# Optimization experiments

Hardware: AMD Instinct MI355X
Metric: run time of the kernel (lower is better)

## Reference

```python
import jax, jax.numpy as jnp
import numpy as np

N_HEAD = 16
NEG_INF = -1e30  # finite mask value, safe for softmax/grad


def setup_inputs() -> dict:
    key = jax.random.key(0)
    k1, k2, k3 = jax.random.split(key, 3)
    B, T, C = 4, 2049, 1024
    x = jax.random.normal(k1, (B, T, C), dtype=jnp.float32)
    W_attn = jax.random.normal(k2, (C, 3 * C), dtype=jnp.float32) * (1.0 / np.sqrt(C))
    W_proj = jax.random.normal(k3, (C, C), dtype=jnp.float32) * (1.0 / np.sqrt(C))
    return {"x": x, "W_attn": W_attn, "W_proj": W_proj}


def reference(x, W_attn, W_proj):
    B, T, C = x.shape
    H = N_HEAD
    D = C // H
    qkv = x @ W_attn                                  # (B, T, 3C)
    q, k, v = jnp.split(qkv, 3, axis=-1)
    q = q.reshape(B, T, H, D).transpose(0, 2, 1, 3)   # (B, H, T, D)
    k = k.reshape(B, T, H, D).transpose(0, 2, 1, 3)
    v = v.reshape(B, T, H, D).transpose(0, 2, 1, 3)
    # hybrid mask: causal tril, but state token (row 0) attends to ALL positions
    mask = jnp.tril(jnp.ones((T, T), dtype=bool))
    mask = mask.at[0, :].set(True)
    scale = 1.0 / np.sqrt(D)
    scores = jnp.einsum('bhtd,bhsd->bhts', q, k) * scale
    scores = jnp.where(mask[None, None, :, :], scores, NEG_INF)
    att = jax.nn.softmax(scores, axis=-1)
    y = jnp.einsum('bhts,bhsd->bhtd', att, v)         # (B, H, T, D)
    y = y.transpose(0, 2, 1, 3).reshape(B, T, C)
    return y @ W_proj
```

## Files before the change

### kernel.cpp

```cpp
#include <hip/hip_runtime.h>

typedef __attribute__((ext_vector_type(8))) __bf16 bf16x8;
typedef __attribute__((ext_vector_type(4))) __bf16 bf16x4;
typedef __attribute__((ext_vector_type(4))) float f32x4;

#define GLDS(g, l) __builtin_amdgcn_global_load_lds( \
    (__attribute__((address_space(1))) void*)(void*)(g), \
    (__attribute__((address_space(3))) void*)(void*)(l), 16, 0, 0)

constexpr int T_REAL = 2049;
constexpr int Tp     = 2112;
constexpr int Mreal  = 8196;
constexpr int Mp     = 8448;
constexpr int GK     = 1024;

constexpr float QSCALE = 0.125f * 1.4426950408889634f;

__global__ __launch_bounds__(256) void cvt_x(const float* __restrict__ x,
                                             __bf16* __restrict__ xb) {
    size_t i = ((size_t)blockIdx.x * 256 + threadIdx.x) * 4;
    float4 v = make_float4(0.f, 0.f, 0.f, 0.f);
    if (i < (size_t)Mreal * GK) v = *(const float4*)(x + i);
    bf16x4 o;
    o.x = (__bf16)v.x; o.y = (__bf16)v.y; o.z = (__bf16)v.z; o.w = (__bf16)v.w;
    *(bf16x4*)(xb + i) = o;
}

__global__ __launch_bounds__(256) void transpose_w(const float* __restrict__ W,
                                                   __bf16* __restrict__ Wt,
                                                   int K, int N) {
    __shared__ float tile[64][65];
    const int n0 = blockIdx.x * 64, k0 = blockIdx.y * 64;
    const int tx = threadIdx.x & 63, ty = threadIdx.x >> 6;
#pragma unroll
    for (int j = 0; j < 16; j++) {
        int rk = ty + j * 4;
        tile[rk][tx] = W[(size_t)(k0 + rk) * N + n0 + tx];
    }
    __syncthreads();
#pragma unroll
    for (int j = 0; j < 16; j++) {
        int rn = ty + j * 4;
        Wt[(size_t)(n0 + rn) * K + k0 + tx] = (__bf16)tile[tx][rn];
    }
}

__global__ __launch_bounds__(256) void transpose_v(const __bf16* __restrict__ v,
                                                   __bf16* __restrict__ vT) {
    __shared__ __bf16 tl[64][72];
    const int bh = blockIdx.y, t0 = blockIdx.x * 64;
    const int tid = threadIdx.x;
    const __bf16* src = v + ((size_t)bh * Tp + t0) * 64;
    {
        const int r = tid >> 3, c = (tid & 7) * 8;
        *(bf16x8*)&tl[r][c]      = *(const bf16x8*)(src + r * 64 + c);
        *(bf16x8*)&tl[r + 32][c] = *(const bf16x8*)(src + (r + 32) * 64 + c);
    }
    __syncthreads();
    __bf16* dst = vT + (size_t)bh * 64 * Tp + t0;
    {
        const int d = tid >> 3, tc = (tid & 7) * 8;
        bf16x8 a, b;
#pragma unroll
        for (int i = 0; i < 8; i++) {
            a[i] = tl[tc + i][d];
            b[i] = tl[tc + i][d + 32];
        }
        *(bf16x8*)(dst + (size_t)d * Tp + tc)        = a;
        *(bf16x8*)(dst + (size_t)(d + 32) * Tp + tc) = b;
    }
}

__global__ __launch_bounds__(512)
void gemm256(const __bf16* __restrict__ A, const __bf16* __restrict__ Bt,
             __bf16* __restrict__ qout, __bf16* __restrict__ kout,
             __bf16* __restrict__ vout) {
    __shared__ __align__(16) __bf16 As[2][16384];
    __shared__ __align__(16) __bf16 Bs[2][16384];

    const int tid = threadIdx.x, lane = tid & 63, w = tid >> 6;
    const int wr = w >> 2, wc = w & 3;
    const int quad = lane >> 4, l15 = lane & 15, l7 = l15 & 7;
    const int m0 = blockIdx.y * 256, n0 = blockIdx.x * 256;

    const int sr = tid >> 3;
    const int sc = ((tid & 7) ^ (sr & 7)) * 8;
    const __bf16* ag = A  + (size_t)(m0 + sr) * GK + sc;
    const __bf16* bg = Bt + (size_t)(n0 + sr) * GK + sc;
    const int ldst = tid * 8;

#define STG_A(T, h) do { const __bf16* s_ = ag + (size_t)(h) * 128 * GK + (T) * 64; \
    GLDS(s_, &As[(T) & 1][(h) * 8192 + ldst]); \
    GLDS(s_ + (size_t)64 * GK, &As[(T) & 1][(h) * 8192 + 4096 + ldst]); } while (0)
#define STG_B(T, h) do { const __bf16* s_ = bg + (size_t)(h) * 128 * GK + (T) * 64; \
    GLDS(s_, &Bs[(T) & 1][(h) * 8192 + ldst]); \
    GLDS(s_ + (size_t)64 * GK, &Bs[(T) & 1][(h) * 8192 + 4096 + ldst]); } while (0)

    f32x4 acc[8][4] = {};
    bf16x8 a[8], b0[4], b1[4];

    STG_A(0, 0); STG_B(0, 1); STG_A(0, 1); STG_B(0, 0); STG_A(1, 0); STG_B(1, 1);
    asm volatile("s_waitcnt vmcnt(4)" ::: "memory");
    __builtin_amdgcn_s_barrier();

    constexpr int NT = GK / 64;

#pragma unroll 1
    for (int T = 0; T < NT; ++T) {
        const int p = T & 1;

#pragma unroll
        for (int f = 0; f < 4; ++f) {
            const int R = f * 32 + wr * 16 + l15;
            a[f * 2 + 0] = *(const bf16x8*)&As[p][R * 64 + ((quad ^ l7) * 8)];
            a[f * 2 + 1] = *(const bf16x8*)&As[p][R * 64 + (((4 + quad) ^ l7) * 8)];
        }
#pragma unroll
        for (int n = 0; n < 2; ++n) {
            const int R = n * 64 + wc * 16 + l15;
            b0[n * 2 + 0] = *(const bf16x8*)&Bs[p][R * 64 + ((quad ^ l7) * 8)];
            b0[n * 2 + 1] = *(const bf16x8*)&Bs[p][R * 64 + (((4 + quad) ^ l7) * 8)];
        }
        if (T + 1 < NT) { STG_A(T + 1, 1); STG_B(T + 1, 0); }
        __builtin_amdgcn_s_barrier();
        asm volatile("s_waitcnt lgkmcnt(0)" ::: "memory");
        __builtin_amdgcn_sched_barrier(0);
        __builtin_amdgcn_s_setprio(1);
#pragma unroll
        for (int f = 0; f < 4; ++f)
#pragma unroll
            for (int n = 0; n < 2; ++n) {
                acc[f][n] = __builtin_amdgcn_mfma_f32_16x16x32_bf16(a[f*2+0], b0[n*2+0], acc[f][n], 0, 0, 0);
                acc[f][n] = __builtin_amdgcn_mfma_f32_16x16x32_bf16(a[f*2+1], b0[n*2+1], acc[f][n], 0, 0, 0);
            }
        __builtin_amdgcn_s_setprio(0);
        __builtin_amdgcn_s_barrier();

#pragma unroll
        for (int n = 0; n < 2; ++n) {
            const int R = 128 + n * 64 + wc * 16 + l15;
            b1[n * 2 + 0] = *(const bf16x8*)&Bs[p][R * 64 + ((quad ^ l7) * 8)];
            b1[n * 2 + 1] = *(const bf16x8*)&Bs[p][R * 64 + (((4 + quad) ^ l7) * 8)];
        }
        __builtin_amdgcn_s_barrier();
        asm volatile("s_waitcnt lgkmcnt(0)" ::: "memory");
        __builtin_amdgcn_sched_barrier(0);
        __builtin_amdgcn_s_setprio(1);
#pragma unroll
        for (int f = 0; f < 4; ++f)
#pragma unroll
            for (int n = 0; n < 2; ++n) {
                acc[f][2+n] = __builtin_amdgcn_mfma_f32_16x16x32_bf16(a[f*2+0], b1[n*2+0], acc[f][2+n], 0, 0, 0);
                acc[f][2+n] = __builtin_amdgcn_mfma_f32_16x16x32_bf16(a[f*2+1], b1[n*2+1], acc[f][2+n], 0, 0, 0);
            }
        __builtin_amdgcn_s_setprio(0);
        __builtin_amdgcn_s_barrier();

#pragma unroll
        for (int f = 0; f < 4; ++f) {
            const int R = 128 + f * 32 + wr * 16 + l15;
            a[f * 2 + 0] = *(const bf16x8*)&As[p][R * 64 + ((quad ^ l7) * 8)];
            a[f * 2 + 1] = *(const bf16x8*)&As[p][R * 64 + (((4 + quad) ^ l7) * 8)];
        }
        if (T + 2 < NT) STG_A(T + 2, 0);
        __builtin_amdgcn_s_barrier();
        asm volatile("s_waitcnt lgkmcnt(0)" ::: "memory");
        __builtin_amdgcn_sched_barrier(0);
        __builtin_amdgcn_s_setprio(1);
#pragma unroll
        for (int f = 0; f < 4; ++f)
#pragma unroll
            for (int n = 0; n < 2; ++n) {
                acc[4+f][2+n] = __builtin_amdgcn_mfma_f32_16x16x32_bf16(a[f*2+0], b1[n*2+0], acc[4+f][2+n], 0, 0, 0);
                acc[4+f][2+n] = __builtin_amdgcn_mfma_f32_16x16x32_bf16(a[f*2+1], b1[n*2+1], acc[4+f][2+n], 0, 0, 0);
            }
        __builtin_amdgcn_s_setprio(0);
        __builtin_amdgcn_s_barrier();

        if (T + 2 < NT) STG_B(T + 2, 1);
        __builtin_amdgcn_s_barrier();
        asm volatile("s_waitcnt lgkmcnt(0)" ::: "memory");
        __builtin_amdgcn_sched_barrier(0);
        __builtin_amdgcn_s_setprio(1);
#pragma unroll
        for (int f = 0; f < 4; ++f)
#pragma unroll
            for (int n = 0; n < 2; ++n) {
                acc[4+f][n] = __builtin_amdgcn_mfma_f32_16x16x32_bf16(a[f*2+0], b0[n*2+0], acc[4+f][n], 0, 0, 0);
                acc[4+f][n] = __builtin_amdgcn_mfma_f32_16x16x32_bf16(a[f*2+1], b0[n*2+1], acc[4+f][n], 0, 0, 0);
            }
        __builtin_amdgcn_s_setprio(0);
        if (T < NT - 2) { asm volatile("s_waitcnt vmcnt(4)" ::: "memory"); }
        else            { asm volatile("s_waitcnt vmcnt(0)" ::: "memory"); }
        __builtin_amdgcn_s_barrier();
    }
#undef STG_A
#undef STG_B

    const int which = n0 >> 10;
    __bf16* op = (which == 0) ? qout : (which == 1) ? kout : vout;
    const float scl = (which == 0) ? QSCALE : 1.0f;
    __bf16* ep = &As[0][0];
    const int rr = tid >> 4, cc = tid & 15;
#pragma unroll
    for (int f = 0; f < 8; ++f) {
        __syncthreads();
#pragma unroll
        for (int n = 0; n < 4; ++n) {
            const int col = (n & 1) * 64 + wc * 16 + (n >> 1) * 128 + l15;
#pragma unroll
            for (int r = 0; r < 4; ++r)
                ep[(wr * 16 + quad * 4 + r) * 264 + col] = (__bf16)(acc[f][n][r] * scl);
        }
        __syncthreads();
        const int m = m0 + (f & 3) * 32 + (f >> 2) * 128 + rr;
        if (m < Mreal) {
            const int b = m / T_REAL;
            const int t = m - b * T_REAL;
#pragma unroll
            for (int g = 0; g < 2; ++g) {
                const int c8 = (cc + g * 16) * 8;
                bf16x8 vv = *(const bf16x8*)&ep[rr * 264 + c8];
                const int gc = n0 + c8;
                const int h = (gc >> 6) & 15;
                *(bf16x8*)&op[((size_t)(b * 16 + h) * Tp + t) * 64 + (gc & 63)] = vv;
            }
        }
    }
}

template <int EPI>
__global__ __launch_bounds__(256)
void gemm128(const __bf16* __restrict__ A, const __bf16* __restrict__ Bt,
             float* __restrict__ outp,
             __bf16* __restrict__ qout, __bf16* __restrict__ kout,
             __bf16* __restrict__ vout) {
    __shared__ __bf16 As[128 * 64];
    __shared__ __bf16 Bs[128 * 64];

    const int tid = threadIdx.x, lane = tid & 63, w = tid >> 6;
    const int wr = w >> 1, wc = w & 1;
    const int quad = lane >> 4, l15 = lane & 15, l7 = l15 & 7;
    const int m0 = blockIdx.y * 128, n0 = blockIdx.x * 128;

    const int row0 = w * 32 + (lane >> 3);
    const int gc8 = ((lane & 7) ^ ((lane >> 3) & 7)) * 8;
    const __bf16* agp = A + (size_t)(m0 + row0) * GK + gc8;
    const __bf16* bgp = Bt + (size_t)(n0 + row0) * GK + gc8;
    __bf16* lap = &As[(w * 256 + lane) * 8];
    __bf16* lbp = &Bs[(w * 256 + lane) * 8];

    f32x4 acc[4][4] = {};

    for (int k0 = 0; k0 < GK; k0 += 64) {
#pragma unroll
        for (int s = 0; s < 4; s++) {
            GLDS(agp + (size_t)s * 8 * GK + k0, lap + s * 512);
            GLDS(bgp + (size_t)s * 8 * GK + k0, lbp + s * 512);
        }
        __syncthreads();
#pragma unroll
        for (int kk = 0; kk < 2; kk++) {
            bf16x8 fa[4], fb[4];
#pragma unroll
            for (int i = 0; i < 4; i++)
                fa[i] = *(const bf16x8*)&As[(wr * 64 + i * 16 + l15) * 64 + (((kk * 4 + quad) ^ l7) * 8)];
#pragma unroll
            for (int j = 0; j < 4; j++)
                fb[j] = *(const bf16x8*)&Bs[(wc * 64 + j * 16 + l15) * 64 + (((kk * 4 + quad) ^ l7) * 8)];
#pragma unroll
            for (int i = 0; i < 4; i++)
#pragma unroll
                for (int j = 0; j < 4; j++)
                    acc[i][j] = __builtin_amdgcn_mfma_f32_16x16x32_bf16(fa[i], fb[j], acc[i][j], 0, 0, 0);
        }
        __syncthreads();
    }

    if constexpr (EPI == 0) {
        const int which = n0 >> 10;
        const int h = ((n0 + wc * 64) >> 6) & 15;
        __bf16* op = (which == 0) ? qout : (which == 1) ? kout : vout;
        const float scl = (which == 0) ? QSCALE : 1.0f;
        __bf16* wls = &As[w * 2048];
#pragma unroll
        for (int p = 0; p < 2; p++) {
            if (p) __syncthreads();
#pragma unroll
            for (int i2 = 0; i2 < 2; i2++)
#pragma unroll
                for (int j = 0; j < 4; j++)
#pragma unroll
                    for (int r = 0; r < 4; r++) {
                        const int lrow = i2 * 16 + quad * 4 + r;
                        const int cX = (j * 2 + (l15 >> 3)) ^ (lrow & 7);
                        wls[lrow * 64 + cX * 8 + (l15 & 7)] =
                            (__bf16)(acc[p * 2 + i2][j][r] * scl);
                    }
            __syncthreads();
#pragma unroll
            for (int it = 0; it < 4; it++) {
                const int lrow = (lane >> 3) + it * 8;
                bf16x8 vv = *(const bf16x8*)&wls[lrow * 64 + (((lane & 7) ^ (lrow & 7)) * 8)];
                const int m = m0 + wr * 64 + p * 32 + lrow;
                if (m < Mreal) {
                    const int b = m / T_REAL;
                    const int t = m - b * T_REAL;
                    *(bf16x8*)&op[(((size_t)(b * 16 + h)) * Tp + t) * 64 + (lane & 7) * 8] = vv;
                }
            }
        }
    } else {
        float* wlf = (float*)&As[0] + w * 1024;
#pragma unroll
        for (int p = 0; p < 4; p++) {
            if (p) __syncthreads();
#pragma unroll
            for (int j = 0; j < 4; j++)
#pragma unroll
                for (int r = 0; r < 4; r++) {
                    const int lrow = quad * 4 + r;
                    const int cX = (j * 4 + (l15 >> 2)) ^ (lrow & 7);
                    wlf[lrow * 64 + cX * 4 + (l15 & 3)] = acc[p][j][r];
                }
            __syncthreads();
#pragma unroll
            for (int it = 0; it < 4; it++) {
                const int lrow = lane >> 2;
                const int c = (lane & 3) + it * 4;
                f32x4 vv = *(const f32x4*)&wlf[lrow * 64 + ((c ^ (lrow & 7)) * 4)];
                const int m = m0 + wr * 64 + p * 16 + lrow;
                if (m < Mreal)
                    *(f32x4*)&outp[(size_t)m * 1024 + n0 + wc * 64 + c * 4] = vv;
            }
        }
    }
}

__global__ __launch_bounds__(512, 6)
void attn(const __bf16* __restrict__ q, const __bf16* __restrict__ kk,
          const __bf16* __restrict__ vT, __bf16* __restrict__ y) {
    __shared__ __bf16 Ks[2][64 * 64];
    __shared__ __bf16 Vs[2][64 * 64];
    __shared__ __bf16 Pq[8][16 * 64];

    static const int QA[17] = {0,31,29,27,25,23,21,19,17,15,13,11,9,7,5,3,1};
    static const int QB[17] = {32,30,28,26,24,22,20,18,16,14,12,10,8,6,4,2,-1};

    const int tid = threadIdx.x, lane = tid & 63, w = tid >> 6;
    const int quad = lane >> 4, l15 = lane & 15;
    const int l7 = l15 & 7;
    const int z = blockIdx.x;
    const int slot = z >> 6;
    const int zz = z & 63;
    const int bh = (zz & 7) * 8 + (zz >> 3);

    const int qtA = QA[slot];
    const int qt = (w < 4) ? qtA : QB[slot];
    const bool active = qt >= 0;
    const int qts = active ? qt : 0;
    const int q0 = qts * 64;
    const int qg = q0 + (w & 3) * 16 + l15;
    const int myNt = (qts == 0) ? 32 : qts;
    const int ntmaxB = (qtA == 0) ? 32 : qtA;

    const __bf16* kgb = kk + (size_t)bh * Tp * 64;
    const __bf16* vgb = vT + (size_t)bh * 64 * Tp;
    const int b = bh >> 4, h = bh & 15;

    const int r0 = tid >> 3;
    const int s0 = ((tid & 7) ^ (r0 & 7)) * 8;
    const int koff = r0 * 64 + s0;
    const int voff = r0 * Tp + s0;

    bf16x8 qa0, qa1;
    {
        const __bf16* qp = q + ((size_t)bh * Tp + qg) * 64 + quad * 8;
        qa0 = *(const bf16x8*)qp;
        qa1 = *(const bf16x8*)(qp + 32);
    }

    f32x4 o[4] = {};
    float mrow = -3e38f, lrow = 0.f;

    GLDS(kgb + koff, &Ks[0][tid * 8]);
    GLDS(vgb + voff, &Vs[0][tid * 8]);

    int cur = 0;
    for (int nt = 0; nt <= ntmaxB; ++nt) {
        __syncthreads();
        if (nt < ntmaxB) {
            GLDS(kgb + (size_t)(nt + 1) * 4096 + koff, &Ks[cur ^ 1][tid * 8]);
            GLDS(vgb + (size_t)(nt + 1) * 64 + voff, &Vs[cur ^ 1][tid * 8]);
        }
        if (active && nt <= myNt) {
            const int kv0 = nt * 64;

            f32x4 st[4];
#pragma unroll
            for (int j = 0; j < 4; j++) {
                const __bf16* krow = &Ks[cur][(j * 16 + l15) * 64];
                bf16x8 klo = *(const bf16x8*)(krow + ((quad ^ l7) * 8));
                bf16x8 khi = *(const bf16x8*)(krow + (((quad + 4) ^ l7) * 8));
                f32x4 zzv = {0.f, 0.f, 0.f, 0.f};
                zzv = __builtin_amdgcn_mfma_f32_16x16x32_bf16(klo, qa0, zzv, 0, 0, 0);
                st[j] = __builtin_amdgcn_mfma_f32_16x16x32_bf16(khi, qa1, zzv, 0, 0, 0);
            }

            if (nt >= qts) {
#pragma unroll
                for (int j = 0; j < 4; j++)
#pragma unroll
                    for (int r = 0; r < 4; r++) {
                        const int kvg = kv0 + j * 16 + quad * 4 + r;
                        const bool valid = (kvg <= qg) || (qg == 0 && kvg < T_REAL);
                        st[j][r] = valid ? st[j][r] : -1e30f;
                    }
            }

            float mx = -3e38f;
#pragma unroll
            for (int j = 0; j < 4; j++)
#pragma unroll
                for (int r = 0; r < 4; r++) mx = fmaxf(mx, st[j][r]);
            mx = fmaxf(mx, __shfl_xor(mx, 16));
            mx = fmaxf(mx, __shfl_xor(mx, 32));
            const float mn = fmaxf(mrow, mx);
            const float alpha = __builtin_amdgcn_exp2f(mrow - mn);
            mrow = mn;

            float rs = 0.f;
            bf16x4 pk[4];
#pragma unroll
            for (int j = 0; j < 4; j++) {
                float p0 = __builtin_amdgcn_exp2f(st[j][0] - mn);
                float p1 = __builtin_amdgcn_exp2f(st[j][1] - mn);
                float p2 = __builtin_amdgcn_exp2f(st[j][2] - mn);
                float p3 = __builtin_amdgcn_exp2f(st[j][3] - mn);
                rs += (p0 + p1) + (p2 + p3);
                pk[j].x = (__bf16)p0; pk[j].y = (__bf16)p1;
                pk[j].z = (__bf16)p2; pk[j].w = (__bf16)p3;
            }
            rs += __shfl_xor(rs, 16);
            rs += __shfl_xor(rs, 32);
            lrow = lrow * alpha + rs;
#pragma unroll
            for (int nf = 0; nf < 4; nf++)
#pragma unroll
                for (int r = 0; r < 4; r++) o[nf][r] *= alpha;

#pragma unroll
            for (int j = 0; j < 4; j++)
                *(bf16x4*)&Pq[w][l15 * 64 + (((2 * j + (quad >> 1)) ^ l7) * 8) + (quad & 1) * 4] = pk[j];

#pragma unroll
            for (int kc = 0; kc < 2; kc++) {
                bf16x8 pb = *(const bf16x8*)&Pq[w][l15 * 64 + (((kc * 4 + quad) ^ l7) * 8)];
#pragma unroll
                for (int nf = 0; nf < 4; nf++) {
                    bf16x8 va = *(const bf16x8*)&Vs[cur][(nf * 16 + l15) * 64 + (((kc * 4 + quad) ^ l7) * 8)];
                    o[nf] = __builtin_amdgcn_mfma_f32_16x16x32_bf16(va, pb, o[nf], 0, 0, 0);
                }
            }
        }
        cur ^= 1;
    }

    if (active && qg < T_REAL) {
        const float inv = 1.0f / lrow;
        __bf16* yp = y + ((size_t)(b * T_REAL + qg)) * 1024 + h * 64 + quad * 4;
#pragma unroll
        for (int nf = 0; nf < 4; nf++) {
            bf16x4 pko;
            pko.x = (__bf16)(o[nf][0] * inv);
            pko.y = (__bf16)(o[nf][1] * inv);
            pko.z = (__bf16)(o[nf][2] * inv);
            pko.w = (__bf16)(o[nf][3] * inv);
            *(bf16x4*)(yp + nf * 16) = pko;
        }
    }
}

extern "C" void kernel_launch(void* const* d_in, const int* in_sizes, int n_in,
                              void* d_out, int out_size, void* d_ws, size_t ws_size,
                              hipStream_t stream) {
    const float* x  = (const float*)d_in[0];
    const float* Wa = (const float*)d_in[1];
    const float* Wp = (const float*)d_in[2];
    float* out = (float*)d_out;

    char* ws = (char*)d_ws;
    constexpr size_t SZ_XB  = (size_t)Mp * GK * 2;
    constexpr size_t SZ_WAT = (size_t)3072 * GK * 2;
    constexpr size_t SZ_WPT = (size_t)1024 * GK * 2;
    constexpr size_t SZ_QK  = (size_t)64 * Tp * 64 * 2;
    __bf16* xb   = (__bf16*)(ws);
    __bf16* WaT  = (__bf16*)(ws + SZ_XB);
    __bf16* WpT  = (__bf16*)(ws + SZ_XB + SZ_WAT);
    __bf16* qb   = (__bf16*)(ws + SZ_XB + SZ_WAT + SZ_WPT);
    __bf16* kb   = (__bf16*)(ws + SZ_XB + SZ_WAT + SZ_WPT + SZ_QK);
    __bf16* vTb  = (__bf16*)(ws + SZ_XB + SZ_WAT + SZ_WPT + 2 * SZ_QK);
    __bf16* shrd = (__bf16*)(ws + SZ_XB + SZ_WAT + SZ_WPT + 3 * SZ_QK);
    __bf16* vpre = shrd;
    __bf16* yb   = shrd;

    cvt_x<<<(Mp * GK) / 1024, 256, 0, stream>>>(x, xb);
    transpose_w<<<dim3(48, 16), 256, 0, stream>>>(Wa, WaT, 1024, 3072);
    transpose_w<<<dim3(16, 16), 256, 0, stream>>>(Wp, WpT, 1024, 1024);

    gemm256<<<dim3(12, 33), 512, 0, stream>>>(xb, WaT, qb, kb, vpre);
    transpose_v<<<dim3(33, 64), 256, 0, stream>>>(vpre, vTb);
    attn<<<1088, 512, 0, stream>>>(qb, kb, vTb, yb);
    gemm128<1><<<dim3(8, 65), 256, 0, stream>>>(yb, WpT, out, nullptr, nullptr, nullptr);
}
```

Before: 278.2 us.

## Remap GEMM blocks per XCD, rebalance attention slots, and skip softmax rescale

After: 297.5 us. 1.07x slower.

```diff
diff --git a/kernel.cpp b/kernel.cpp
--- a/kernel.cpp
+++ b/kernel.cpp
@@ -81,7 +81,12 @@
     const int tid = threadIdx.x, lane = tid & 63, w = tid >> 6;
     const int wr = w >> 2, wc = w & 3;
     const int quad = lane >> 4, l15 = lane & 15, l7 = l15 & 7;
-    const int m0 = blockIdx.y * 256, n0 = blockIdx.x * 256;
+
+    constexpr int NWG = 396, QW = NWG / 8, RW = NWG % 8;
+    const int zb = blockIdx.x;
+    const int xcd = zb & 7, lin = zb >> 3;
+    const int wg = (xcd < RW ? xcd * (QW + 1) : RW * (QW + 1) + (xcd - RW) * QW) + lin;
+    const int m0 = (wg / 12) * 256, n0 = (wg % 12) * 256;
 
     const int sr = tid >> 3;
     const int sc = ((tid & 7) ^ (sr & 7)) * 8;
@@ -337,32 +342,25 @@
     }
 }
 
-__global__ __launch_bounds__(512, 6)
+__global__ __launch_bounds__(512, 8)
 void attn(const __bf16* __restrict__ q, const __bf16* __restrict__ kk,
           const __bf16* __restrict__ vT, __bf16* __restrict__ y) {
     __shared__ __bf16 Ks[2][64 * 64];
     __shared__ __bf16 Vs[2][64 * 64];
-    __shared__ __bf16 Pq[8][16 * 64];
-
-    static const int QA[17] = {0,31,29,27,25,23,21,19,17,15,13,11,9,7,5,3,1};
-    static const int QB[17] = {32,30,28,26,24,22,20,18,16,14,12,10,8,6,4,2,-1};
+    __shared__ __bf16 Pq[8][16 * 32];
+
+    static const int TBL[16] = {0,1,2,3,7,6,5,4,8,9,10,11,15,14,13,12};
+    static const int QA[16]  = {0,31,29,27,25,23,21,19,17,15,13,11,9,7,5,3};
+    static const int QB[16]  = {32,30,28,26,24,22,20,18,16,14,12,10,8,6,4,2};
 
     const int tid = threadIdx.x, lane = tid & 63, w = tid >> 6;
     const int quad = lane >> 4, l15 = lane & 15;
     const int l7 = l15 & 7;
     const int z = blockIdx.x;
-    const int slot = z >> 6;
+    const int sp = TBL[z >> 6];
     const int zz = z & 63;
     const int bh = (zz & 7) * 8 + (zz >> 3);
-
-    const int qtA = QA[slot];
-    const int qt = (w < 4) ? qtA : QB[slot];
-    const bool active = qt >= 0;
-    const int qts = active ? qt : 0;
-    const int q0 = qts * 64;
-    const int qg = q0 + (w & 3) * 16 + l15;
-    const int myNt = (qts == 0) ? 32 : qts;
-    const int ntmaxB = (qtA == 0) ? 32 : qtA;
+    const int npass = (sp == 15) ? 2 : 1;
 
     const __bf16* kgb = kk + (size_t)bh * Tp * 64;
     const __bf16* vgb = vT + (size_t)bh * 64 * Tp;
@@ -373,110 +371,127 @@
     const int koff = r0 * 64 + s0;
     const int voff = r0 * Tp + s0;
 
-    bf16x8 qa0, qa1;
-    {
-        const __bf16* qp = q + ((size_t)bh * Tp + qg) * 64 + quad * 8;
-        qa0 = *(const bf16x8*)qp;
-        qa1 = *(const bf16x8*)(qp + 32);
-    }
-
-    f32x4 o[4] = {};
-    float mrow = -3e38f, lrow = 0.f;
+    const int pswz = (((l15 >> 1) & 3) << 1) ^ ((l15 >> 3) << 2);
 
     GLDS(kgb + koff, &Ks[0][tid * 8]);
     GLDS(vgb + voff, &Vs[0][tid * 8]);
-
     int cur = 0;
-    for (int nt = 0; nt <= ntmaxB; ++nt) {
-        __syncthreads();
-        if (nt < ntmaxB) {
-            GLDS(kgb + (size_t)(nt + 1) * 4096 + koff, &Ks[cur ^ 1][tid * 8]);
-            GLDS(vgb + (size_t)(nt + 1) * 64 + voff, &Vs[cur ^ 1][tid * 8]);
-        }
-        if (active && nt <= myNt) {
-            const int kv0 = nt * 64;
-
-            f32x4 st[4];
-#pragma unroll
-            for (int j = 0; j < 4; j++) {
-                const __bf16* krow = &Ks[cur][(j * 16 + l15) * 64];
-                bf16x8 klo = *(const bf16x8*)(krow + ((quad ^ l7) * 8));
-                bf16x8 khi = *(const bf16x8*)(krow + (((quad + 4) ^ l7) * 8));
-                f32x4 zzv = {0.f, 0.f, 0.f, 0.f};
-                zzv = __builtin_amdgcn_mfma_f32_16x16x32_bf16(klo, qa0, zzv, 0, 0, 0);
-                st[j] = __builtin_amdgcn_mfma_f32_16x16x32_bf16(khi, qa1, zzv, 0, 0, 0);
-            }
-
-            if (nt >= qts) {
+
+#pragma unroll 1
+    for (int pass = 0; pass < npass; ++pass) {
+        const int qt = (pass == 0) ? ((w < 4) ? QA[sp] : QB[sp])
+                                   : ((w < 4) ? -1 : 1);
+        const bool active = qt >= 0;
+        const int qts = active ? qt : 0;
+        const int qg = qts * 64 + (w & 3) * 16 + l15;
+        const int myNt = (qts == 0) ? 32 : qts;
+        const int ntB = (pass == 0) ? ((sp == 0) ? 32 : QA[sp]) : 1;
+
+        bf16x8 qa0, qa1;
+        {
+            const __bf16* qp = q + ((size_t)bh * Tp + qg) * 64 + quad * 8;
+            qa0 = *(const bf16x8*)qp;
+            qa1 = *(const bf16x8*)(qp + 32);
+        }
+        f32x4 o[4] = {};
+        float mrow = -3e38f, lrow = 0.f;
+
+#pragma unroll 1
+        for (int nt = 0; nt <= ntB; ++nt) {
+            __syncthreads();
+            if (nt < ntB) {
+                GLDS(kgb + (size_t)(nt + 1) * 4096 + koff, &Ks[cur ^ 1][tid * 8]);
+                GLDS(vgb + (size_t)(nt + 1) * 64 + voff, &Vs[cur ^ 1][tid * 8]);
+            } else if (pass + 1 < npass) {
+                GLDS(kgb + koff, &Ks[cur ^ 1][tid * 8]);
+                GLDS(vgb + voff, &Vs[cur ^ 1][tid * 8]);
+            }
+            if (active && nt <= myNt) {
+                const int kv0 = nt * 64;
+
+                f32x4 st[4];
+#pragma unroll
+                for (int j = 0; j < 4; j++) {
+                    const __bf16* krow = &Ks[cur][(j * 16 + l15) * 64];
+                    bf16x8 klo = *(const bf16x8*)(krow + ((quad ^ l7) * 8));
+                    bf16x8 khi = *(const bf16x8*)(krow + (((quad + 4) ^ l7) * 8));
+                    f32x4 zzv = {0.f, 0.f, 0.f, 0.f};
+                    zzv = __builtin_amdgcn_mfma_f32_16x16x32_bf16(klo, qa0, zzv, 0, 0, 0);
+                    st[j] = __builtin_amdgcn_mfma_f32_16x16x32_bf16(khi, qa1, zzv, 0, 0, 0);
+                }
+
+                if (nt >= qts) {
+#pragma unroll
+                    for (int j = 0; j < 4; j++)
+#pragma unroll
+                        for (int r = 0; r < 4; r++) {
+                            const int kvg = kv0 + j * 16 + quad * 4 + r;
+                            const bool valid = (kvg <= qg) || (qg == 0 && kvg < T_REAL);
+                            st[j][r] = valid ? st[j][r] : -1e30f;
+                        }
+                }
+
+                float mx = -3e38f;
 #pragma unroll
                 for (int j = 0; j < 4; j++)
 #pragma unroll
-                    for (int r = 0; r < 4; r++) {
-                        const int kvg = kv0 + j * 16 + quad * 4 + r;
-                        const bool valid = (kvg <= qg) || (qg == 0 && kvg < T_REAL);
-                        st[j][r] = valid ? st[j][r] : -1e30f;
+                    for (int r = 0; r < 4; r++) mx = fmaxf(mx, st[j][r]);
+                mx = fmaxf(mx, __shfl_xor(mx, 16));
+                mx = fmaxf(mx, __shfl_xor(mx, 32));
+                if (!__all(mx - mrow <= 8.0f)) {
+                    const float mn = fmaxf(mrow, mx);
+                    const float alpha = __builtin_amdgcn_exp2f(mrow - mn);
+                    mrow = mn;
+                    lrow *= alpha;
+#pragma unroll
+                    for (int nf = 0; nf < 4; nf++)
+#pragma unroll
+                        for (int r = 0; r < 4; r++) o[nf][r] *= alpha;
+                }
+
+                float rs = 0.f;
+                bf16x4 pk[4];
+#pragma unroll
+                for (int j = 0; j < 4; j++) {
+                    float p0 = __builtin_amdgcn_exp2f(st[j][0] - mrow);
+                    float p1 = __builtin_amdgcn_exp2f(st[j][1] - mrow);
+                    float p2 = __builtin_amdgcn_exp2f(st[j][2] - mrow);
+                    float p3 = __builtin_amdgcn_exp2f(st[j][3] - mrow);
+                    rs += (p0 + p1) + (p2 + p3);
+                    pk[j].x = (__bf16)p0; pk[j].y = (__bf16)p1;
+                    pk[j].z = (__bf16)p2; pk[j].w = (__bf16)p3;
+                }
+                rs += __shfl_xor(rs, 16);
+                rs += __shfl_xor(rs, 32);
+                lrow += rs;
+
+#pragma unroll
+                for (int h2 = 0; h2 < 2; ++h2) {
+                    *(bf16x4*)&Pq[w][l15 * 32 + (((0 + quad) ^ pswz) * 4)] = pk[2 * h2];
+                    *(bf16x4*)&Pq[w][l15 * 32 + (((4 + quad) ^ pswz) * 4)] = pk[2 * h2 + 1];
+                    bf16x8 pb = *(const bf16x8*)&Pq[w][l15 * 32 + (((quad * 2) ^ pswz) * 4)];
+#pragma unroll
+                    for (int nf = 0; nf < 4; nf++) {
+                        bf16x8 va = *(const bf16x8*)&Vs[cur][(nf * 16 + l15) * 64 + (((h2 * 4 + quad) ^ l7) * 8)];
+                        o[nf] = __builtin_amdgcn_mfma_f32_16x16x32_bf16(va, pb, o[nf], 0, 0, 0);
                     }
-            }
-
-            float mx = -3e38f;
-#pragma unroll
-            for (int j = 0; j < 4; j++)
-#pragma unroll
-                for (int r = 0; r < 4; r++) mx = fmaxf(mx, st[j][r]);
-            mx = fmaxf(mx, __shfl_xor(mx, 16));
-            mx = fmaxf(mx, __shfl_xor(mx, 32));
-            const float mn = fmaxf(mrow, mx);
-            const float alpha = __builtin_amdgcn_exp2f(mrow - mn);
-            mrow = mn;
-
-            float rs = 0.f;
-            bf16x4 pk[4];
-#pragma unroll
-            for (int j = 0; j < 4; j++) {
-                float p0 = __builtin_amdgcn_exp2f(st[j][0] - mn);
-                float p1 = __builtin_amdgcn_exp2f(st[j][1] - mn);
-                float p2 = __builtin_amdgcn_exp2f(st[j][2] - mn);
-                float p3 = __builtin_amdgcn_exp2f(st[j][3] - mn);
-                rs += (p0 + p1) + (p2 + p3);
-                pk[j].x = (__bf16)p0; pk[j].y = (__bf16)p1;
-                pk[j].z = (__bf16)p2; pk[j].w = (__bf16)p3;
-            }
-            rs += __shfl_xor(rs, 16);
-            rs += __shfl_xor(rs, 32);
-            lrow = lrow * alpha + rs;
-#pragma unroll
-            for (int nf = 0; nf < 4; nf++)
-#pragma unroll
-                for (int r = 0; r < 4; r++) o[nf][r] *= alpha;
-
-#pragma unroll
-            for (int j = 0; j < 4; j++)
-                *(bf16x4*)&Pq[w][l15 * 64 + (((2 * j + (quad >> 1)) ^ l7) * 8) + (quad & 1) * 4] = pk[j];
-
-#pragma unroll
-            for (int kc = 0; kc < 2; kc++) {
-                bf16x8 pb = *(const bf16x8*)&Pq[w][l15 * 64 + (((kc * 4 + quad) ^ l7) * 8)];
-#pragma unroll
-                for (int nf = 0; nf < 4; nf++) {
-                    bf16x8 va = *(const bf16x8*)&Vs[cur][(nf * 16 + l15) * 64 + (((kc * 4 + quad) ^ l7) * 8)];
-                    o[nf] = __builtin_amdgcn_mfma_f32_16x16x32_bf16(va, pb, o[nf], 0, 0, 0);
-                }
-            }
-        }
-        cur ^= 1;
-    }
-
-    if (active && qg < T_REAL) {
-        const float inv = 1.0f / lrow;
-        __bf16* yp = y + ((size_t)(b * T_REAL + qg)) * 1024 + h * 64 + quad * 4;
-#pragma unroll
-        for (int nf = 0; nf < 4; nf++) {
-            bf16x4 pko;
-            pko.x = (__bf16)(o[nf][0] * inv);
-            pko.y = (__bf16)(o[nf][1] * inv);
-            pko.z = (__bf16)(o[nf][2] * inv);
-            pko.w = (__bf16)(o[nf][3] * inv);
-            *(bf16x4*)(yp + nf * 16) = pko;
+                }
+            }
+            cur ^= 1;
+        }
+
+        if (active && qg < T_REAL) {
+            const float inv = 1.0f / lrow;
+            __bf16* yp = y + ((size_t)(b * T_REAL + qg)) * 1024 + h * 64 + quad * 4;
+#pragma unroll
+            for (int nf = 0; nf < 4; nf++) {
+                bf16x4 pko;
+                pko.x = (__bf16)(o[nf][0] * inv);
+                pko.y = (__bf16)(o[nf][1] * inv);
+                pko.z = (__bf16)(o[nf][2] * inv);
+                pko.w = (__bf16)(o[nf][3] * inv);
+                *(bf16x4*)(yp + nf * 16) = pko;
+            }
         }
     }
 }
@@ -508,8 +523,8 @@
     transpose_w<<<dim3(48, 16), 256, 0, stream>>>(Wa, WaT, 1024, 3072);
     transpose_w<<<dim3(16, 16), 256, 0, stream>>>(Wp, WpT, 1024, 1024);
 
-    gemm256<<<dim3(12, 33), 512, 0, stream>>>(xb, WaT, qb, kb, vpre);
+    gemm256<<<396, 512, 0, stream>>>(xb, WaT, qb, kb, vpre);
     transpose_v<<<dim3(33, 64), 256, 0, stream>>>(vpre, vTb);
-    attn<<<1088, 512, 0, stream>>>(qb, kb, vTb, yb);
+    attn<<<1024, 512, 0, stream>>>(qb, kb, vTb, yb);
     gemm128<1><<<dim3(8, 65), 256, 0, stream>>>(yb, WpT, out, nullptr, nullptr, nullptr);
 }
```
